# Kernel optimization log

Measured on AMD Instinct MI355X. Metric: run time of the kernel, lower is better.

Reference implementation:

```python
import jax, jax.numpy as jnp
import numpy as np

HID = 512      # out_channels / HR2O hidden_dim
CIN = 2048     # conv1 input channels (Cf + Cx)
DEPTH = 3
EPS = 1e-5     # GroupNorm eps


def conv2d(x, w, pad):
    return jax.lax.conv_general_dilated(
        x, w, window_strides=(1, 1), padding=[(pad, pad), (pad, pad)],
        dimension_numbers=('NCHW', 'OIHW', 'NCHW'))


def hr2o(x, wq, wk, wv, wm, gamma, beta):
    # x: [N, C, H, W]
    q = conv2d(x, wq, 1)
    k = conv2d(x, wk, 1)
    v = conv2d(x, wv, 1)
    # (query.unsqueeze(1) * key.unsqueeze(0)).sum(2) / sqrt(C) -> [N, N, H, W]
    att = jnp.einsum('qchw,kchw->qkhw', q, k) / jnp.sqrt(jnp.float32(HID))
    att = jax.nn.softmax(att, axis=1)  # softmax over key dim
    # (att.unsqueeze(2) * value).sum(1) -> [N, C, H, W]
    vf = jnp.einsum('qkhw,kchw->qchw', att, v)
    # GroupNorm(1, C): normalize over (C, H, W), per-channel affine
    mu = jnp.mean(vf, axis=(1, 2, 3), keepdims=True)
    var = jnp.var(vf, axis=(1, 2, 3), keepdims=True)
    vf = (vf - mu) * jax.lax.rsqrt(var + EPS)
    vf = vf * gamma[None, :, None, None] + beta[None, :, None, None]
    vf = jax.nn.relu(vf)
    vf = conv2d(vf, wm, 1)
    # Dropout(0.2) is identity in eval mode
    return x + vf


def setup_inputs() -> dict:
    key = jax.random.key(0)
    ks = jax.random.split(key, 12)
    N, B = 32, 8
    Cx, Cf, H, W = 1024, 1024, 16, 16
    s = 0.02
    return {
        'x': jax.random.normal(ks[0], (N, Cx, 4, 7, 7), jnp.float32),
        'feat': jax.random.normal(ks[1], (B, Cf, 1, H, W), jnp.float32),
        'rois': jax.random.randint(ks[2], (N, 5), 0, B, jnp.int32),
        'w1': jax.random.normal(ks[3], (HID, CIN, 1, 1), jnp.float32) * s,
        'w2': jax.random.normal(ks[4], (HID, HID, 3, 3), jnp.float32) * s,
        'wq': jax.random.normal(ks[5], (DEPTH, HID, HID, 3, 3), jnp.float32) * s,
        'wk': jax.random.normal(ks[6], (DEPTH, HID, HID, 3, 3), jnp.float32) * s,
        'wv': jax.random.normal(ks[7], (DEPTH, HID, HID, 3, 3), jnp.float32) * s,
        'wm': jax.random.normal(ks[8], (DEPTH, HID, HID, 3, 3), jnp.float32) * s,
        'gamma': jnp.ones((DEPTH, HID), jnp.float32),
        'beta': jnp.zeros((DEPTH, HID), jnp.float32),
    }


def reference(x, feat, rois, w1, w2, wq, wk, wv, wm, gamma, beta):
    n, cx = x.shape[0], x.shape[1]
    # AdaptiveMaxPool3d(1) -> [N, Cx, 1, 1, 1]
    xp = jnp.max(x, axis=(2, 3, 4), keepdims=True)
    h, w = feat.shape[-2], feat.shape[-1]
    roi_inds = rois[:, 0].astype(jnp.int32)
    roi_gfeat = feat[roi_inds]                              # [N, Cf, 1, H, W]
    x_tile = jnp.broadcast_to(xp, (n, cx, 1, h, w))         # repeat(1,1,1,h,w)
    nf = jnp.concatenate([roi_gfeat, x_tile], axis=1)[:, :, 0]  # squeeze(2)
    nf = jax.nn.relu(conv2d(nf, w1, 0))                     # 1x1 conv
    nf = jax.nn.relu(conv2d(nf, w2, 0))                     # 3x3 conv, no pad
    for i in range(DEPTH):
        nf = hr2o(nf, wq[i], wk[i], wv[i], wm[i], gamma[i], beta[i])
    nf = jnp.mean(nf, axis=(2, 3), keepdims=True)[:, :, None]  # gap -> [N,C,1,1,1]
    return jnp.concatenate([xp, nf], axis=1)                # [N, Cx+HID, 1, 1, 1]
```

## Files before the change

### kernel.cpp

```cpp
#include <hip/hip_runtime.h>


typedef __attribute__((ext_vector_type(8))) short bhalf8;
typedef __attribute__((ext_vector_type(4))) float floatx4;

#define ACT_N 131072
#define W3SZ  2359296

__device__ inline float b2f(unsigned short u) {
  union { unsigned int i; float f; } x; x.i = ((unsigned int)u) << 16; return x.f;
}
__device__ inline unsigned short f2b(float f) {
  union { float f; unsigned int i; } x; x.f = f;
  return (unsigned short)((x.i + 0x7FFFu + ((x.i >> 16) & 1u)) >> 16);
}
__device__ inline void gload_lds16(const unsigned short* g, bhalf8* l) {
  __builtin_amdgcn_global_load_lds(
      (const __attribute__((address_space(1))) unsigned int*)(const void*)g,
      (__attribute__((address_space(3))) unsigned int*)(void*)l, 16, 0, 0);
}
template <int N> __device__ inline void waitvm() {
  asm volatile("s_waitcnt vmcnt(%0)" :: "i"(N) : "memory");
}
__device__ inline void SB() { __builtin_amdgcn_sched_barrier(0); }
__device__ inline void endphase() {
  SB(); waitvm<0>();
  __builtin_amdgcn_s_barrier();
  SB();
}

__global__ void pool_max_kernel(const float* __restrict__ x, float* __restrict__ xp,
                                float* __restrict__ out) {
  int tid = threadIdx.x;
  int wid = blockIdx.x * 4 + (tid >> 6);
  int lane = tid & 63;
  int n = wid >> 10, c = wid & 1023;
  const float* p = x + (size_t)wid * 196;
  float v = -3.4e38f;
  v = fmaxf(v, p[lane]);
  v = fmaxf(v, p[lane + 64]);
  v = fmaxf(v, p[lane + 128]);
  if (lane < 4) v = fmaxf(v, p[lane + 192]);
#pragma unroll
  for (int off = 32; off >= 1; off >>= 1) v = fmaxf(v, __shfl_xor(v, off));
  if (lane == 0) { xp[wid] = v; out[(size_t)n * 1536 + c] = v; }
}

__global__ void bias1_kernel(const float* __restrict__ w1, const float* __restrict__ xp,
                             float* __restrict__ bias1) {
  int tid = threadIdx.x;
  int wid = blockIdx.x * 4 + (tid >> 6);
  int lane = tid & 63;
  int n = wid >> 9, o = wid & 511;
  const float* wr = w1 + (size_t)o * 2048 + 1024;
  const float* xr = xp + (size_t)n * 1024;
  float s = 0.f;
#pragma unroll
  for (int r = 0; r < 16; r++) { int c = lane + r * 64; s += wr[c] * xr[c]; }
#pragma unroll
  for (int off = 32; off >= 1; off >>= 1) s += __shfl_xor(s, off);
  if (lane == 0) bias1[wid] = s;
}

__global__ __launch_bounds__(256) void wprep3_kernel(
    const float* __restrict__ w2, const float* __restrict__ wq,
    const float* __restrict__ wk, const float* __restrict__ wv,
    const float* __restrict__ wm, unsigned short* __restrict__ Wg2) {
  int ks = blockIdx.x, ot = blockIdx.y, tid = blockIdx.z;
  int t = threadIdx.x;
  const float* src;
  if (tid == 0) src = w2;
  else {
    int d = (tid - 1) >> 2, r = (tid - 1) & 3;
    src = (r == 0 ? wq : r == 1 ? wk : r == 2 ? wv : wm) + (size_t)d * W3SZ;
  }
  __shared__ unsigned short S[64 * 288];
  const float* sb = src + (size_t)ot * 64 * 4608 + (size_t)ks * 288;
  for (int j = 0; j < 72; j++) {
    int flat = j * 256 + t;
    int o = flat / 288, ci = flat % 288;
    S[flat] = f2b(sb[(size_t)o * 4608 + ci]);
  }
  __syncthreads();
  unsigned short* dst = Wg2 + (((size_t)(tid * 8 + ot) * 16 + ks) * 2304) * 8;
#pragma unroll
  for (int s = 0; s < 9; s++) {
    int u = t + s * 256;
    int g = u / 768, rem = u % 768;
    int rl = rem >> 6, o = rem & 63;
    int dh = rl >> 2, kg = rl & 3;
    int t9src = dh * 3 + g;
    bhalf8 v;
#pragma unroll
    for (int j = 0; j < 8; j++) v[j] = (short)S[o * 288 + (kg * 8 + j) * 9 + t9src];
    *(bhalf8*)(dst + (size_t)u * 8) = v;
  }
}

__global__ void w1prep_kernel(const float* __restrict__ w1, unsigned short* __restrict__ W1g) {
  int ks = blockIdx.x, ot = blockIdx.y, t = threadIdx.x;
  int kg = t >> 6, o = t & 63;
  const float* s = w1 + (size_t)(ot * 64 + o) * 2048 + ks * 32 + kg * 8;
  bhalf8 v;
#pragma unroll
  for (int j = 0; j < 8; j++) v[j] = (short)f2b(s[j]);
  *(bhalf8*)(W1g + (((size_t)ot * 32 + ks) * 256 + t) * 8) = v;
}

__global__ __launch_bounds__(256) void ftprep_kernel(
    const float* __restrict__ feat, unsigned short* __restrict__ featT) {
  int img = blockIdx.z, c0 = blockIdx.y * 64, p0 = blockIdx.x * 64;
  int t = threadIdx.x;
  int a = t >> 6, b = t & 63;
  __shared__ float S[64][65];
#pragma unroll
  for (int j = 0; j < 16; j++) {
    int r = a * 16 + j;
    S[r][b] = feat[((size_t)img * 1024 + c0 + r) * 256 + p0 + b];
  }
  __syncthreads();
#pragma unroll
  for (int j = 0; j < 16; j++) {
    int pl = a * 16 + j;
    featT[((size_t)img * 256 + p0 + pl) * 1024 + c0 + b] = f2b(S[b][pl]);
  }
}

template <int TAPS, int KTOT, int WAVES, int NREP, int PSPLIT,
          bool RELU, bool ADD, bool BIAS, bool VALID>
__global__ __launch_bounds__(WAVES * 64, 2) void conv_mfma_kernel(
    const unsigned short* __restrict__ Xg, const int* __restrict__ rois,
    const unsigned short* __restrict__ Wg, const float* __restrict__ bias,
    unsigned short* __restrict__ Out) {
  constexpr int THREADS = WAVES * 64;
  constexpr int NK = KTOT / 32;
  static_assert(PSPLIT * WAVES * NREP * 16 == 256, "p coverage");
  static_assert((NK & 1) == 0, "even NK");

  int n = blockIdx.x;
  int ot = blockIdx.y / PSPLIT;
  int pq = blockIdx.y % PSPLIT;
  int t = threadIdx.x;
  int wv = t >> 6, l = t & 63, l15 = l & 15, l4 = l >> 4;
  int pbase = (pq * WAVES + wv) * (NREP * 16);
  const unsigned short* xb =
      Xg + (rois ? (size_t)rois[n * 5] * 256 * KTOT : (size_t)n * 256 * KTOT);
  floatx4 acc[4][NREP] = {};

  if constexpr (TAPS == 9) {
    constexpr int LX = 1024 / THREADS;
    static_assert(768 % THREADS == 0 && 1024 % THREADS == 0, "stage div");
    __shared__ bhalf8 Xs[2][1024];
    __shared__ bhalf8 Wl[3][768];

    auto stageX = [&](int xbuf, int ks) {
#pragma unroll
      for (int i = 0; i < LX; i++) {
        int base = i * THREADS + wv * 64;
        int u = base + l;
        int p = u & 255, kg = u >> 8;
        gload_lds16(xb + (size_t)p * KTOT + ks * 32 + kg * 8, &Xs[xbuf][base]);
      }
    };
    auto stageW = [&](int wbuf, int ks, int g) {
      const unsigned short* wb =
          Wg + (((size_t)ot * NK + ks) * 2304 + g * 768) * 8;
#pragma unroll
      for (int i = 0; i < 768 / THREADS; i++) {
        int base = i * THREADS + wv * 64;
        gload_lds16(wb + (size_t)(base + l) * 8, &Wl[wbuf][base]);
      }
    };
    auto ldregs = [&](bhalf8 (&BW)[NREP + 2], bhalf8 (&A)[12], int ks, int g) {
      const bhalf8* X = Xs[ks & 1];
#pragma unroll
      for (int w10 = 0; w10 < NREP + 2; w10++)
        BW[w10] = X[l4 * 256 + ((pbase + w10 * 16 + l15 + g) & 255)];
      const bhalf8* W = Wl[g];
#pragma unroll
      for (int dh = 0; dh < 3; dh++)
#pragma unroll
        for (int of = 0; of < 4; of++)
          A[dh * 4 + of] = W[(dh * 4 + l4) * 64 + of * 16 + l15];
    };
    auto domfma = [&](bhalf8 (&BW)[NREP + 2], bhalf8 (&A)[12]) {
      __builtin_amdgcn_s_setprio(1);
#pragma unroll
      for (int dh = 0; dh < 3; dh++)
#pragma unroll
        for (int of = 0; of < 4; of++)
#pragma unroll
          for (int pf = 0; pf < NREP; pf++)
            acc[of][pf] = __builtin_amdgcn_mfma_f32_16x16x32_bf16(
                A[dh * 4 + of], BW[pf + dh], acc[of][pf], 0, 0, 0);
      __builtin_amdgcn_s_setprio(0);
    };

    bhalf8 BW0[NREP + 2], A0[12], BW1[NREP + 2], A1[12];

    stageX(0, 0); stageW(0, 0, 0);
    endphase();
    ldregs(BW0, A0, 0, 0); SB();
    stageW(1, 0, 1); stageX(1, 1);
    endphase();

    for (int ks = 0; ks < NK; ks += 2) {
      ldregs(BW1, A1, ks, 1); SB();
      stageW(2, ks, 2); SB();
      domfma(BW0, A0); endphase();
      ldregs(BW0, A0, ks, 2); SB();
      stageW(0, ks + 1, 0); SB();
      domfma(BW1, A1); endphase();
      ldregs(BW1, A1, ks + 1, 0); SB();
      stageW(1, ks + 1, 1);
      if (ks + 2 < NK) stageX(ks & 1, ks + 2);
      SB();
      domfma(BW0, A0); endphase();
      ldregs(BW0, A0, ks + 1, 1); SB();
      stageW(2, ks + 1, 2); SB();
      domfma(BW1, A1); endphase();
      ldregs(BW1, A1, ks + 1, 2); SB();
      if (ks + 2 < NK) stageW(0, ks + 2, 0);
      SB();
      domfma(BW0, A0); endphase();
      if (ks + 2 < NK) { ldregs(BW0, A0, ks + 2, 0); SB(); }
      if (ks + 2 < NK) stageW(1, ks + 2, 1);
      if (ks + 3 < NK) stageX((ks + 1) & 1, ks + 3);
      SB();
      domfma(BW1, A1); endphase();
    }
  } else {
    constexpr int LX = 1024 / THREADS;
    static_assert(256 % THREADS == 0 && 1024 % THREADS == 0, "stage div");
    __shared__ bhalf8 Xs[3][1024];
    __shared__ bhalf8 Wl[3][256];

    auto stage1 = [&](int b, int ks) {
#pragma unroll
      for (int i = 0; i < LX; i++) {
        int base = i * THREADS + wv * 64;
        int u = base + l;
        int p = u & 255, kg = u >> 8;
        gload_lds16(xb + (size_t)p * KTOT + ks * 32 + kg * 8, &Xs[b][base]);
      }
      const unsigned short* wb = Wg + (((size_t)ot * NK + ks) * 256) * 8;
#pragma unroll
      for (int i = 0; i < 256 / THREADS; i++) {
        int base = i * THREADS + wv * 64;
        gload_lds16(wb + (size_t)(base + l) * 8, &Wl[b][base]);
      }
    };
    auto ldregs1 = [&](bhalf8 (&B)[NREP], bhalf8 (&A)[4], int ks) {
      const bhalf8* X = Xs[ks % 3];
#pragma unroll
      for (int pf = 0; pf < NREP; pf++)
        B[pf] = X[l4 * 256 + ((pbase + pf * 16 + l15) & 255)];
      const bhalf8* W = Wl[ks % 3];
#pragma unroll
      for (int of = 0; of < 4; of++) A[of] = W[l4 * 64 + of * 16 + l15];
    };
    auto domfma1 = [&](bhalf8 (&B)[NREP], bhalf8 (&A)[4]) {
      __builtin_amdgcn_s_setprio(1);
#pragma unroll
      for (int of = 0; of < 4; of++)
#pragma unroll
        for (int pf = 0; pf < NREP; pf++)
          acc[of][pf] = __builtin_amdgcn_mfma_f32_16x16x32_bf16(
              A[of], B[pf], acc[of][pf], 0, 0, 0);
      __builtin_amdgcn_s_setprio(0);
    };

    bhalf8 B0[NREP], A0[4], B1[NREP], A1[4];
    stage1(0, 0);
    endphase();
    ldregs1(B0, A0, 0); SB();
    stage1(1, 1);
    endphase();
    for (int ks = 0; ks < NK; ks += 2) {
      ldregs1(B1, A1, ks + 1); SB();
      if (ks + 2 < NK) stage1((ks + 2) % 3, ks + 2);
      SB();
      domfma1(B0, A0); endphase();
      if (ks + 2 < NK) { ldregs1(B0, A0, ks + 2); SB(); }
      if (ks + 3 < NK) stage1((ks + 3) % 3, ks + 3);
      SB();
      domfma1(B1, A1); endphase();
    }
  }

#pragma unroll
  for (int of = 0; of < 4; of++) {
    int og = ot * 64 + of * 16 + l4 * 4;
    int tensor = og >> 9, ol = og & 511;
#pragma unroll
    for (int pf = 0; pf < NREP; pf++) {
      int p = pbase + pf * 16 + l15;
      int po = p;
      if (VALID) {
        int h = p >> 4, w = p & 15;
        if (h >= 14 || w >= 14) continue;
        po = (h + 1) * 16 + (w + 1);
      }
      unsigned short* dp = Out + (((size_t)tensor * 32 + n) * 256 + po) * 512 + ol;
      float vv[4];
#pragma unroll
      for (int r2 = 0; r2 < 4; r2++) vv[r2] = acc[of][pf][r2];
      if (BIAS) {
#pragma unroll
        for (int r2 = 0; r2 < 4; r2++) vv[r2] += bias[(size_t)n * 512 + ol + r2];
      }
      if (ADD) {
        ushort4 old = *(const ushort4*)dp;
        vv[0] += b2f(old.x); vv[1] += b2f(old.y); vv[2] += b2f(old.z); vv[3] += b2f(old.w);
      }
      if (RELU) {
#pragma unroll
        for (int r2 = 0; r2 < 4; r2++) vv[r2] = fmaxf(vv[r2], 0.f);
      }
      ushort4 st = { f2b(vv[0]), f2b(vv[1]), f2b(vv[2]), f2b(vv[3]) };
      *(ushort4*)dp = st;
    }
  }
}

__global__ __launch_bounds__(256) void vtrans_kernel(
    const unsigned short* __restrict__ v, unsigned short* __restrict__ vt) {
  int ppc = blockIdx.x;
  int pp = (ppc / 14 + 1) * 16 + ppc % 14 + 1;
  int t = threadIdx.x;
  __shared__ unsigned short S[32 * 512];
#pragma unroll
  for (int i = 0; i < 8; i++) {
    int u = i * 256 + t;
    int kn = u >> 6, c8 = (u & 63) * 8;
    *(bhalf8*)&S[kn * 512 + c8] = *(const bhalf8*)(v + ((size_t)kn * 256 + pp) * 512 + c8);
  }
  __syncthreads();
#pragma unroll
  for (int half = 0; half < 2; half++) {
    int c = half * 256 + t;
    unsigned int col[16];
#pragma unroll
    for (int j = 0; j < 16; j++)
      col[j] = (unsigned int)S[(2 * j) * 512 + c] |
               ((unsigned int)S[(2 * j + 1) * 512 + c] << 16);
    unsigned short* dst = vt + ((size_t)ppc * 512 + c) * 32;
#pragma unroll
    for (int j = 0; j < 4; j++) {
      uint4 P = { col[j * 4], col[j * 4 + 1], col[j * 4 + 2], col[j * 4 + 3] };
      *(uint4*)(dst + j * 8) = P;
    }
  }
}

__global__ __launch_bounds__(64) void attfused_kernel(
    const unsigned short* __restrict__ q, const unsigned short* __restrict__ k,
    const unsigned short* __restrict__ vt, unsigned short* __restrict__ out,
    float* __restrict__ gnpart) {
  int pp = blockIdx.x;
  int h = pp >> 4, w = pp & 15;
  int l = threadIdx.x, l15 = l & 15, l4 = l >> 4;
  if (h < 1 || h > 14 || w < 1 || w > 14) {
    uint4 z = {0u, 0u, 0u, 0u};
#pragma unroll
    for (int qn = 0; qn < 32; qn++)
      *(uint4*)(out + ((size_t)qn * 256 + pp) * 512 + l * 8) = z;
    return;
  }
  int ppc = (h - 1) * 14 + (w - 1);

  floatx4 sc[2][2] = {};
#pragma unroll
  for (int kb = 0; kb < 16; kb++) {
    bhalf8 A[2], B[2];
#pragma unroll
    for (int of = 0; of < 2; of++)
      A[of] = *(const bhalf8*)(k + ((size_t)(of * 16 + l15) * 256 + pp) * 512 + kb * 32 + l4 * 8);
#pragma unroll
    for (int pf = 0; pf < 2; pf++)
      B[pf] = *(const bhalf8*)(q + ((size_t)(pf * 16 + l15) * 256 + pp) * 512 + kb * 32 + l4 * 8);
#pragma unroll
    for (int of = 0; of < 2; of++)
#pragma unroll
      for (int pf = 0; pf < 2; pf++)
        sc[of][pf] = __builtin_amdgcn_mfma_f32_16x16x32_bf16(A[of], B[pf], sc[of][pf], 0, 0, 0);
  }

  __shared__ unsigned short p_lds[32 * 32];
  const float scale = 0.044194173824159216f;
#pragma unroll
  for (int pf = 0; pf < 2; pf++) {
    float v8[8];
    float m = -3.4e38f;
#pragma unroll
    for (int of = 0; of < 2; of++)
#pragma unroll
      for (int r = 0; r < 4; r++) {
        float x = sc[of][pf][r] * scale;
        v8[of * 4 + r] = x;
        m = fmaxf(m, x);
      }
    m = fmaxf(m, __shfl_xor(m, 16));
    m = fmaxf(m, __shfl_xor(m, 32));
    float s = 0.f;
#pragma unroll
    for (int i = 0; i < 8; i++) { v8[i] = __expf(v8[i] - m); s += v8[i]; }
    s += __shfl_xor(s, 16);
    s += __shfl_xor(s, 32);
    float inv = 1.f / s;
#pragma unroll
    for (int of = 0; of < 2; of++) {
      ushort4 pk = { f2b(v8[of * 4 + 0] * inv), f2b(v8[of * 4 + 1] * inv),
                     f2b(v8[of * 4 + 2] * inv), f2b(v8[of * 4 + 3] * inv) };
      *(ushort4*)&p_lds[(pf * 16 + l15) * 32 + of * 16 + l4 * 4] = pk;
    }
  }

  bhalf8 PB[2];
#pragma unroll
  for (int qf = 0; qf < 2; qf++)
    PB[qf] = *(const bhalf8*)&p_lds[(qf * 16 + l15) * 32 + l4 * 8];
  float gs[2] = {0.f, 0.f}, gss[2] = {0.f, 0.f};
  const unsigned short* vtb = vt + (size_t)ppc * 512 * 32;
#pragma unroll
  for (int chunk = 0; chunk < 4; chunk++) {
    bhalf8 VA[8];
#pragma unroll
    for (int co = 0; co < 8; co++)
      VA[co] = *(const bhalf8*)(vtb + (size_t)(chunk * 128 + co * 16 + l15) * 32 + l4 * 8);
#pragma unroll
    for (int co = 0; co < 8; co++)
#pragma unroll
      for (int qf = 0; qf < 2; qf++) {
        floatx4 pa = __builtin_amdgcn_mfma_f32_16x16x32_bf16(
            VA[co], PB[qf], (floatx4){0.f, 0.f, 0.f, 0.f}, 0, 0, 0);
        float x0 = pa[0], x1 = pa[1], x2 = pa[2], x3 = pa[3];
        gs[qf] += x0 + x1 + x2 + x3;
        gss[qf] += x0 * x0 + x1 * x1 + x2 * x2 + x3 * x3;
        ushort4 st = { f2b(x0), f2b(x1), f2b(x2), f2b(x3) };
        int qn = qf * 16 + l15;
        int c = chunk * 128 + co * 16 + l4 * 4;
        *(ushort4*)(out + ((size_t)qn * 256 + pp) * 512 + c) = st;
      }
  }
#pragma unroll
  for (int qf = 0; qf < 2; qf++) {
    gs[qf] += __shfl_xor(gs[qf], 16);  gs[qf] += __shfl_xor(gs[qf], 32);
    gss[qf] += __shfl_xor(gss[qf], 16); gss[qf] += __shfl_xor(gss[qf], 32);
  }
  if (l4 == 0) {
#pragma unroll
    for (int qf = 0; qf < 2; qf++) {
      int qn = qf * 16 + l15;
      gnpart[((size_t)ppc * 32 + qn) * 2]     = gs[qf];
      gnpart[((size_t)ppc * 32 + qn) * 2 + 1] = gss[qf];
    }
  }
}

__global__ __launch_bounds__(256) void gnapply3_kernel(
    unsigned short* __restrict__ x, const float* __restrict__ gnpart,
    const float* __restrict__ gamma, const float* __restrict__ beta) {
  int n = blockIdx.y, half = blockIdx.x, t = threadIdx.x;
  float s = 0.f, ss = 0.f;
  if (t < 196) {
    s  = gnpart[((size_t)t * 32 + n) * 2];
    ss = gnpart[((size_t)t * 32 + n) * 2 + 1];
  }
#pragma unroll
  for (int off = 32; off >= 1; off >>= 1) { s += __shfl_xor(s, off); ss += __shfl_xor(ss, off); }
  __shared__ float sm[8];
  int wv = t >> 6, ln = t & 63;
  if (ln == 0) { sm[wv] = s; sm[4 + wv] = ss; }
  __syncthreads();
  float S = sm[0] + sm[1] + sm[2] + sm[3];
  float SS = sm[4] + sm[5] + sm[6] + sm[7];
  const float M = 512.f * 196.f;
  float mu = S / M;
  float var = SS / M - mu * mu;
  float inv = rsqrtf(var + 1e-5f);
  int c2 = t * 2;
  unsigned short* xb = x + (size_t)n * ACT_N;
  float g0 = gamma[c2], g1 = gamma[c2 + 1];
  float be0 = beta[c2], be1 = beta[c2 + 1];
  for (int i = 0; i < 98; i++) {
    int ppc = half * 98 + i;
    int pp = (ppc / 14 + 1) * 16 + ppc % 14 + 1;
    unsigned int vv = *(unsigned int*)(xb + pp * 512 + c2);
    float a = (b2f((unsigned short)vv) - mu) * inv * g0 + be0;
    float b = (b2f((unsigned short)(vv >> 16)) - mu) * inv * g1 + be1;
    a = fmaxf(a, 0.f); b = fmaxf(b, 0.f);
    *(unsigned int*)(xb + pp * 512 + c2) =
        (unsigned int)f2b(a) | ((unsigned int)f2b(b) << 16);
  }
}

__global__ void fmean2_kernel(const unsigned short* __restrict__ x, float* __restrict__ out) {
  int n = blockIdx.x, t = threadIdx.x;
  const unsigned short* xb = x + (size_t)n * ACT_N;
  float s0 = 0.f, s1 = 0.f;
  for (int i = 0; i < 196; i++) {
    int pp = (i / 14 + 1) * 16 + (i % 14) + 1;
    unsigned int vv = *(const unsigned int*)(xb + pp * 512 + t * 2);
    s0 += b2f((unsigned short)vv);
    s1 += b2f((unsigned short)(vv >> 16));
  }
  out[(size_t)n * 1536 + 1024 + t * 2]     = s0 * (1.f / 196.f);
  out[(size_t)n * 1536 + 1024 + t * 2 + 1] = s1 * (1.f / 196.f);
}

extern "C" void kernel_launch(void* const* d_in, const int* in_sizes, int n_in,
                              void* d_out, int out_size, void* d_ws, size_t ws_size,
                              hipStream_t stream) {
  const float* x     = (const float*)d_in[0];
  const float* feat  = (const float*)d_in[1];
  const int*   rois  = (const int*)d_in[2];
  const float* w1    = (const float*)d_in[3];
  const float* w2    = (const float*)d_in[4];
  const float* wq    = (const float*)d_in[5];
  const float* wk    = (const float*)d_in[6];
  const float* wv    = (const float*)d_in[7];
  const float* wm    = (const float*)d_in[8];
  const float* gamma = (const float*)d_in[9];
  const float* beta  = (const float*)d_in[10];
  float* out = (float*)d_out;

  float* wsf   = (float*)d_ws;
  float* xp    = wsf;
  float* bias1 = xp + 32768;
  float* stats = bias1 + 16384;
  float* attf  = stats + 64;
  unsigned short* ub    = (unsigned short*)(attf + 262144);
  unsigned short* featT = ub;
  unsigned short* W1g   = featT + 2097152;
  unsigned short* Wg2   = W1g + 524288;
  unsigned short* bufq  = Wg2 + 30670848;
  unsigned short* bufk  = bufq + 4194304;
  unsigned short* bufv  = bufk + 4194304;
  unsigned short* bufx  = bufv + 4194304;
  unsigned short* vt    = (unsigned short*)d_ws;
  float* gnpart = (float*)(bufx + 4194304);

  hipMemsetAsync(bufx, 0, (size_t)4194304 * 2, stream);

  pool_max_kernel<<<8192, 256, 0, stream>>>(x, xp, out);
  bias1_kernel<<<4096, 256, 0, stream>>>(w1, xp, bias1);
  wprep3_kernel<<<dim3(16, 8, 13), 256, 0, stream>>>(w2, wq, wk, wv, wm, Wg2);
  w1prep_kernel<<<dim3(32, 8), 256, 0, stream>>>(w1, W1g);
  ftprep_kernel<<<dim3(4, 16, 8), 256, 0, stream>>>(feat, featT);

  conv_mfma_kernel<1, 1024, 4, 4, 1, true, false, true, false>
      <<<dim3(32, 8), 256, 0, stream>>>(featT, rois, W1g, bias1, bufq);
  conv_mfma_kernel<9, 512, 4, 4, 1, true, false, false, true>
      <<<dim3(32, 8), 256, 0, stream>>>(bufq, nullptr, Wg2, nullptr, bufx);

  for (int d = 0; d < 3; d++) {
    conv_mfma_kernel<9, 512, 4, 4, 1, false, false, false, true>
        <<<dim3(32, 24), 256, 0, stream>>>(bufx, nullptr,
            Wg2 + (size_t)(1 + 4 * d) * W3SZ, nullptr, bufq);
    vtrans_kernel<<<196, 256, 0, stream>>>(bufv, vt);
    attfused_kernel<<<256, 64, 0, stream>>>(bufq, bufk, vt, bufq, gnpart);
    gnapply3_kernel<<<dim3(2, 32), 256, 0, stream>>>(bufq, gnpart,
        gamma + d * 512, beta + d * 512);
    conv_mfma_kernel<9, 512, 4, 4, 1, false, true, false, true>
        <<<dim3(32, 8), 256, 0, stream>>>(bufq, nullptr,
            Wg2 + (size_t)(4 + 4 * d) * W3SZ, nullptr, bufx);
  }

  fmean2_kernel<<<32, 256, 0, stream>>>(bufx, out);
}
```

Baseline: 681.5 us.

## Use 128-output-channel tiles for fused QKV conv to double activation reuse

Adds a dedicated QKV conv kernel that computes 128 output channels per block (2x2 wave split over channels and pixels), halving the grid and the number of times each input tile is staged. The weight prepack switches to a 128-channel row layout, and the generic conv kernel's weight staging is re-indexed to read its 64-channel half of that layout. This cuts redundant activation loads and LDS staging but raises per-wave accumulator register use and leaves fewer blocks for occupancy.

```diff
diff --git a/kernel.cpp b/kernel.cpp
--- a/kernel.cpp
+++ b/kernel.cpp
@@ -66,7 +66,7 @@
     const float* __restrict__ w2, const float* __restrict__ wq,
     const float* __restrict__ wk, const float* __restrict__ wv,
     const float* __restrict__ wm, unsigned short* __restrict__ Wg2) {
-  int ks = blockIdx.x, ot = blockIdx.y, tid = blockIdx.z;
+  int ks = blockIdx.x, ot2 = blockIdx.y, tid = blockIdx.z;
   int t = threadIdx.x;
   const float* src;
   if (tid == 0) src = w2;
@@ -74,20 +74,20 @@
     int d = (tid - 1) >> 2, r = (tid - 1) & 3;
     src = (r == 0 ? wq : r == 1 ? wk : r == 2 ? wv : wm) + (size_t)d * W3SZ;
   }
-  __shared__ unsigned short S[64 * 288];
-  const float* sb = src + (size_t)ot * 64 * 4608 + (size_t)ks * 288;
-  for (int j = 0; j < 72; j++) {
+  __shared__ unsigned short S[128 * 288];
+  const float* sb = src + (size_t)ot2 * 128 * 4608 + (size_t)ks * 288;
+  for (int j = 0; j < 144; j++) {
     int flat = j * 256 + t;
     int o = flat / 288, ci = flat % 288;
     S[flat] = f2b(sb[(size_t)o * 4608 + ci]);
   }
   __syncthreads();
-  unsigned short* dst = Wg2 + (((size_t)(tid * 8 + ot) * 16 + ks) * 2304) * 8;
-#pragma unroll
-  for (int s = 0; s < 9; s++) {
+  unsigned short* dst = Wg2 + (((size_t)(tid * 4 + ot2) * 16 + ks) * 4608) * 8;
+#pragma unroll
+  for (int s = 0; s < 18; s++) {
     int u = t + s * 256;
-    int g = u / 768, rem = u % 768;
-    int rl = rem >> 6, o = rem & 63;
+    int g = u / 1536, rem = u % 1536;
+    int rl = rem >> 7, o = rem & 127;
     int dh = rl >> 2, kg = rl & 3;
     int t9src = dh * 3 + g;
     bhalf8 v;
@@ -123,6 +123,103 @@
   for (int j = 0; j < 16; j++) {
     int pl = a * 16 + j;
     featT[((size_t)img * 256 + p0 + pl) * 1024 + c0 + b] = f2b(S[b][pl]);
+  }
+}
+
+__global__ __launch_bounds__(256) void conv_mfma8_kernel(
+    const unsigned short* __restrict__ Xg, const unsigned short* __restrict__ Wg,
+    unsigned short* __restrict__ Out) {
+  constexpr int NK = 16;
+  __shared__ bhalf8 Xs[2][1024];
+  __shared__ bhalf8 Wl[2][1536];
+
+  int n = blockIdx.x;
+  int ot2 = blockIdx.y;
+  int t = threadIdx.x;
+  int wv = t >> 6, l = t & 63, l15 = l & 15, l4 = l >> 4;
+  int wo = wv >> 1, wp = wv & 1;
+  int pbase = wp * 128;
+  const unsigned short* xb = Xg + (size_t)n * 256 * 512;
+  const unsigned short* wB = Wg + (size_t)ot2 * NK * 4608 * 8;
+  floatx4 acc[4][8] = {};
+
+  auto stageX = [&](int xbuf, int ks) {
+#pragma unroll
+    for (int i = 0; i < 4; i++) {
+      int base = i * 256 + wv * 64;
+      int u = base + l;
+      int p = u & 255, kg = u >> 8;
+      gload_lds16(xb + (size_t)p * 512 + ks * 32 + kg * 8, &Xs[xbuf][base]);
+    }
+  };
+  auto stageW = [&](int wbuf, int ks, int g) {
+    const unsigned short* wp8 = wB + ((size_t)ks * 4608 + g * 1536) * 8;
+#pragma unroll
+    for (int i = 0; i < 6; i++) {
+      int base = i * 256 + wv * 64;
+      gload_lds16(wp8 + (size_t)(base + l) * 8, &Wl[wbuf][base]);
+    }
+  };
+  auto computeG = [&](int xbuf, int wbuf, int g) {
+    const bhalf8* X = Xs[xbuf];
+    const bhalf8* W = Wl[wbuf];
+    bhalf8 BW[10];
+#pragma unroll
+    for (int w10 = 0; w10 < 10; w10++)
+      BW[w10] = X[l4 * 256 + ((pbase + w10 * 16 + l15 + g) & 255)];
+#pragma unroll
+    for (int dh = 0; dh < 3; dh++) {
+      bhalf8 A[4];
+#pragma unroll
+      for (int of = 0; of < 4; of++)
+        A[of] = W[(dh * 4 + l4) * 128 + wo * 64 + of * 16 + l15];
+      __builtin_amdgcn_s_setprio(1);
+#pragma unroll
+      for (int of = 0; of < 4; of++)
+#pragma unroll
+        for (int pf = 0; pf < 8; pf++)
+          acc[of][pf] = __builtin_amdgcn_mfma_f32_16x16x32_bf16(
+              A[of], BW[pf + dh], acc[of][pf], 0, 0, 0);
+      __builtin_amdgcn_s_setprio(0);
+    }
+  };
+
+  stageW(0, 0, 0); stageX(0, 0);
+  endphase();
+
+  for (int ks = 0; ks < NK; ks += 2) {
+    stageW(1, ks, 1); SB();
+    computeG(ks & 1, 0, 0); endphase();
+    stageW(0, ks, 2); stageX((ks + 1) & 1, ks + 1); SB();
+    computeG(ks & 1, 1, 1); endphase();
+    stageW(1, ks + 1, 0); SB();
+    computeG(ks & 1, 0, 2); endphase();
+    stageW(0, ks + 1, 1); SB();
+    computeG((ks + 1) & 1, 1, 0); endphase();
+    stageW(1, ks + 1, 2);
+    if (ks + 2 < NK) stageX(ks & 1, ks + 2);
+    SB();
+    computeG((ks + 1) & 1, 0, 1); endphase();
+    if (ks + 2 < NK) stageW(0, ks + 2, 0);
+    SB();
+    computeG((ks + 1) & 1, 1, 2); endphase();
+  }
+
+#pragma unroll
+  for (int of = 0; of < 4; of++) {
+    int og = ot2 * 128 + wo * 64 + of * 16 + l4 * 4;
+    int tensor = og >> 9, ol = og & 511;
+#pragma unroll
+    for (int pf = 0; pf < 8; pf++) {
+      int p = pbase + pf * 16 + l15;
+      int h = p >> 4, w = p & 15;
+      if (h >= 14 || w >= 14) continue;
+      int po = (h + 1) * 16 + (w + 1);
+      unsigned short* dp = Out + (((size_t)tensor * 32 + n) * 256 + po) * 512 + ol;
+      ushort4 st = { f2b(acc[of][pf][0]), f2b(acc[of][pf][1]),
+                     f2b(acc[of][pf][2]), f2b(acc[of][pf][3]) };
+      *(ushort4*)dp = st;
+    }
   }
 }
 
@@ -152,6 +249,7 @@
     static_assert(768 % THREADS == 0 && 1024 % THREADS == 0, "stage div");
     __shared__ bhalf8 Xs[2][1024];
     __shared__ bhalf8 Wl[3][768];
+    const int ot2 = ot >> 1, oh = ot & 1;
 
     auto stageX = [&](int xbuf, int ks) {
 #pragma unroll
@@ -164,11 +262,12 @@
     };
     auto stageW = [&](int wbuf, int ks, int g) {
       const unsigned short* wb =
-          Wg + (((size_t)ot * NK + ks) * 2304 + g * 768) * 8;
+          Wg + (((size_t)ot2 * NK + ks) * 4608 + g * 1536) * 8;
 #pragma unroll
       for (int i = 0; i < 768 / THREADS; i++) {
         int base = i * THREADS + wv * 64;
-        gload_lds16(wb + (size_t)(base + l) * 8, &Wl[wbuf][base]);
+        int rl = base >> 6;
+        gload_lds16(wb + (size_t)(rl * 128 + oh * 64 + l) * 8, &Wl[wbuf][base]);
       }
     };
     auto ldregs = [&](bhalf8 (&BW)[NREP + 2], bhalf8 (&A)[12], int ks, int g) {
@@ -545,7 +644,7 @@
 
   pool_max_kernel<<<8192, 256, 0, stream>>>(x, xp, out);
   bias1_kernel<<<4096, 256, 0, stream>>>(w1, xp, bias1);
-  wprep3_kernel<<<dim3(16, 8, 13), 256, 0, stream>>>(w2, wq, wk, wv, wm, Wg2);
+  wprep3_kernel<<<dim3(16, 4, 13), 256, 0, stream>>>(w2, wq, wk, wv, wm, Wg2);
   w1prep_kernel<<<dim3(32, 8), 256, 0, stream>>>(w1, W1g);
   ftprep_kernel<<<dim3(4, 16, 8), 256, 0, stream>>>(feat, featT);
 
@@ -555,9 +654,8 @@
       <<<dim3(32, 8), 256, 0, stream>>>(bufq, nullptr, Wg2, nullptr, bufx);
 
   for (int d = 0; d < 3; d++) {
-    conv_mfma_kernel<9, 512, 4, 4, 1, false, false, false, true>
-        <<<dim3(32, 24), 256, 0, stream>>>(bufx, nullptr,
-            Wg2 + (size_t)(1 + 4 * d) * W3SZ, nullptr, bufq);
+    conv_mfma8_kernel<<<dim3(32, 12), 256, 0, stream>>>(
+        bufx, Wg2 + (size_t)(1 + 4 * d) * W3SZ, bufq);
     vtrans_kernel<<<196, 256, 0, stream>>>(bufv, vt);
     attfused_kernel<<<256, 64, 0, stream>>>(bufq, bufk, vt, bufq, gnpart);
     gnapply3_kernel<<<dim3(2, 32), 256, 0, stream>>>(bufq, gnpart,
```

After: 864.7 us. 26.9% more time.
